# Optimization experiments

Measured on AMD Instinct MI355X. Metric: run time of the kernel, lower is better.

Reference implementation:

```python
import jax, jax.numpy as jnp
import numpy as np

EPS = 1e-5
NEG = -10000.0


def rel_shift(x):
    # x: [B, H, T1, T2] with T2 = 2*T1 - 1 -> returns [B, H, T1, T1]
    B, H, T1, T2 = x.shape
    x = jnp.pad(x, ((0, 0), (0, 0), (0, 0), (1, 0)))        # [B,H,T1,T2+1]
    x = x.reshape(B, H, T2 + 1, T1)[:, :, 1:, :].reshape(B, H, T1, T2)
    return x[:, :, :, : T2 // 2 + 1]


def setup_inputs() -> dict:
    key = jax.random.key(0)
    B, C, T, H = 4, 512, 1024, 8
    ks = jax.random.split(key, 16)
    s = 0.02
    inp = {
        "x": jax.random.normal(ks[0], (B, C, T), jnp.float32),
        "pos_emb": jax.random.normal(ks[1], (1, C, 2 * T - 1), jnp.float32),
        "x_mask": jnp.ones((B, 1, T), jnp.float32),
        "gamma": jnp.ones((C,), jnp.float32),
        "beta": jnp.zeros((C,), jnp.float32),
        "Wq": jax.random.normal(ks[2], (C, C), jnp.float32) * s,
        "bq": jnp.zeros((C,), jnp.float32),
        "Wk": jax.random.normal(ks[3], (C, C), jnp.float32) * s,
        "bk": jnp.zeros((C,), jnp.float32),
        "Wv": jax.random.normal(ks[4], (C, C), jnp.float32) * s,
        "bv": jnp.zeros((C,), jnp.float32),
        "Wp": jax.random.normal(ks[5], (C, C), jnp.float32) * s,
        "u_bias": jax.random.normal(ks[6], (H, C // H), jnp.float32) * s,
        "v_bias": jax.random.normal(ks[7], (H, C // H), jnp.float32) * s,
        "Wo": jax.random.normal(ks[8], (C, C), jnp.float32) * s,
        "bo": jnp.zeros((C,), jnp.float32),
    }
    return inp


def reference(x, pos_emb, x_mask, gamma, beta, Wq, bq, Wk, bk, Wv, bv, Wp,
              u_bias, v_bias, Wo, bo):
    B, C, T = x.shape
    H, Dh = u_bias.shape

    # channel LayerNorm (axis=1)
    mean = jnp.mean(x, axis=1, keepdims=True)
    var = jnp.mean((x - mean) ** 2, axis=1, keepdims=True)
    xn = (x - mean) * jax.lax.rsqrt(var + EPS)
    xn = xn * gamma[None, :, None] + beta[None, :, None]

    conv1x1 = lambda W, b, z: jnp.einsum('oc,bct->bot', W, z) + b[None, :, None]
    q = conv1x1(Wq, bq, xn).reshape(B, H, Dh, T)
    k = conv1x1(Wk, bk, xn).reshape(B, H, Dh, T)
    v = conv1x1(Wv, bv, xn).reshape(B, H, Dh, T)
    p = jnp.einsum('oc,xct->xot', Wp, pos_emb)          # [1, C, 2T-1], no bias
    p = p.reshape(p.shape[0], H, Dh, -1)[0]             # [H, Dh, 2T-1]

    content = jnp.einsum('bhdt,bhds->bhts', q + u_bias[None, :, :, None], k)
    pos = jnp.einsum('bhdt,hds->bhts', q + v_bias[None, :, :, None], p)
    pos = rel_shift(pos)                                 # [B, H, T, T]

    score = (content + pos) / jnp.sqrt(jnp.float32(C))
    attn_mask = x_mask[:, :, None, :] * x_mask[:, :, :, None]  # [B,1,T,T]
    score = jnp.where(attn_mask == 0, NEG, score)
    attn = jax.nn.softmax(score, axis=-1)

    # context[d,t] = sum_s v[d,s] * attn[s,t]
    ctx = jnp.einsum('bhds,bhst->bhdt', v, attn).reshape(B, C, T)
    return jnp.einsum('oc,bct->bot', Wo, ctx) + bo[None, :, None]
```

## Files before the change

kernel.cpp:

```cpp
#include <hip/hip_runtime.h>
#include <hip/hip_bf16.h>
#include <cmath>

typedef unsigned short u16;
typedef __bf16 bf16_t;
typedef bf16_t bf16x8 __attribute__((ext_vector_type(8)));
typedef float f32x4 __attribute__((ext_vector_type(4)));
typedef u16 u16x8 __attribute__((ext_vector_type(8)));

#define MFMA16(A,B,C) __builtin_amdgcn_mfma_f32_16x16x32_bf16(A,B,C,0,0,0)

#define CB 512
#define TT 1024
#define NH 8
#define DH 64
#define ALPHA (0.044194173824159216f * 1.4426950408889634f)
#define MASKL 14426.950408889634f

static __device__ __forceinline__ u16 f2b(float f) {
  unsigned u = __float_as_uint(f);
  unsigned r = u + 0x7FFFu + ((u >> 16) & 1u);
  return (u16)(r >> 16);
}
static __device__ __forceinline__ float b2f(u16 u) {
  return __uint_as_float(((unsigned)u) << 16);
}
static __device__ __forceinline__ bf16x8 ldb8(const u16* p) {
  return *reinterpret_cast<const bf16x8*>(p);
}

__global__ __launch_bounds__(256)
void convert5(const float* __restrict__ Wq, const float* __restrict__ Wk,
              const float* __restrict__ Wv, const float* __restrict__ Wp,
              const float* __restrict__ Wo,
              u16* __restrict__ Wstk, u16* __restrict__ WoB)
{
  int i = blockIdx.x * 256 + threadIdx.x;
  int sel = i >> 15, loc = i & 32767;
  const float* src = (sel == 0) ? Wq : (sel == 1) ? Wk : (sel == 2) ? Wv
                   : (sel == 3) ? Wp : Wo;
  const float4 a = ((const float4*)src)[loc * 2 + 0];
  const float4 b = ((const float4*)src)[loc * 2 + 1];
  u16x8 o;
  o[0] = f2b(a.x); o[1] = f2b(a.y); o[2] = f2b(a.z); o[3] = f2b(a.w);
  o[4] = f2b(b.x); o[5] = f2b(b.y); o[6] = f2b(b.z); o[7] = f2b(b.w);
  u16* dst = (sel < 4) ? (Wstk + (size_t)i * 8) : (WoB + (size_t)loc * 8);
  *(u16x8*)dst = o;
}

__global__ __launch_bounds__(256)
void transpose_pe(const float* __restrict__ pe, u16* __restrict__ posT)
{
  __shared__ float tile[64][65];
  int j0 = blockIdx.x * 64, c0 = blockIdx.y * 64;
  for (int e = threadIdx.x; e < 4096; e += 256) {
    int cc = e >> 6, jj = e & 63;
    int j = j0 + jj;
    tile[jj][cc] = (j < 2047) ? pe[(size_t)(c0 + cc) * 2047 + j] : 0.f;
  }
  __syncthreads();
  for (int e = threadIdx.x; e < 4096; e += 256) {
    int jj = e >> 6, cc = e & 63;
    posT[(size_t)(j0 + jj) * 512 + c0 + cc] = f2b(tile[jj][cc]);
  }
}

__global__ __launch_bounds__(256)
void ln_kernel(const float* __restrict__ x, const float* __restrict__ gamma,
               const float* __restrict__ beta, u16* __restrict__ xnT)
{
  __shared__ float sred[8][33], ssred[8][33];
  int tl = threadIdx.x & 31, cg = threadIdx.x >> 5;
  int t = blockIdx.x * 32 + tl;
  int b = blockIdx.y;
  const float* xb = x + (size_t)b * CB * TT + t;
  float s = 0.f, ss = 0.f;
  for (int c = cg * 64; c < cg * 64 + 64; ++c) {
    float v = xb[(size_t)c * TT];
    s += v; ss += v * v;
  }
  sred[cg][tl] = s; ssred[cg][tl] = ss;
  __syncthreads();
  float S = 0.f, SS = 0.f;
  #pragma unroll
  for (int g = 0; g < 8; ++g) { S += sred[g][tl]; SS += ssred[g][tl]; }
  float mean = S * (1.f / 512.f);
  float var = SS * (1.f / 512.f) - mean * mean;
  float rstd = rsqrtf(var + 1e-5f);
  u16* orow = xnT + ((size_t)b * TT + t) * CB;
  for (int c8 = 0; c8 < 8; ++c8) {
    int c = cg * 64 + c8 * 8;
    u16x8 o;
    #pragma unroll
    for (int j = 0; j < 8; ++j) {
      float v = xb[(size_t)(c + j) * TT];
      o[j] = f2b((v - mean) * rstd * gamma[c + j] + beta[c + j]);
    }
    *(u16x8*)(orow + c) = o;
  }
}

template<int K, int OMODE>
__global__ __launch_bounds__(256)
void gemm2(const u16* __restrict__ A, const u16* __restrict__ XT,
           long xStride, long oStride, int Nout,
           const float* __restrict__ b0, void* __restrict__ outv)
{
  const int tid = threadIdx.x, w = tid >> 6, lane = tid & 63;
  const int ln16 = lane & 15, kg = lane >> 4;
  const int wm = w & 1, wn = w >> 1;
  const int m0 = blockIdx.y * 64 + wm * 32;
  const int n0 = blockIdx.x * 128 + wn * 64;
  const int z = blockIdx.z;
  const u16* Ar = A + (size_t)(m0 + ln16) * K + kg * 8;
  const u16* Br = XT + (size_t)z * xStride + (size_t)(n0 + ln16) * K + kg * 8;
  f32x4 acc[2][4] = {};
  #pragma unroll 2
  for (int ks = 0; ks < K / 32; ++ks) {
    bf16x8 a[2], bb[4];
    #pragma unroll
    for (int mt = 0; mt < 2; ++mt) a[mt] = ldb8(Ar + (size_t)mt * 16 * K + ks * 32);
    #pragma unroll
    for (int nt = 0; nt < 4; ++nt) bb[nt] = ldb8(Br + (size_t)nt * 16 * K + ks * 32);
    #pragma unroll
    for (int mt = 0; mt < 2; ++mt)
      #pragma unroll
      for (int nt = 0; nt < 4; ++nt)
        acc[mt][nt] = MFMA16(a[mt], bb[nt], acc[mt][nt]);
  }
  float add[2][4];
  #pragma unroll
  for (int mt = 0; mt < 2; ++mt)
    #pragma unroll
    for (int jr = 0; jr < 4; ++jr)
      add[mt][jr] = b0 ? b0[m0 + mt * 16 + kg * 4 + jr] : 0.f;
  #pragma unroll
  for (int mt = 0; mt < 2; ++mt)
    #pragma unroll
    for (int nt = 0; nt < 4; ++nt) {
      const int n = n0 + nt * 16 + ln16;
      if constexpr (OMODE == 0) {
        float* out = (float*)outv;
        #pragma unroll
        for (int jr = 0; jr < 4; ++jr)
          out[(size_t)z * oStride + (size_t)(m0 + mt * 16 + kg * 4 + jr) * Nout + n] =
              acc[mt][nt][jr] + add[mt][jr];
      } else {
        const int m_low = m0 + mt * 16;
        const size_t o = (size_t)z * oStride +
                         ((size_t)(m_low >> 6) * Nout + n) * 64 + (m_low & 63) + kg * 4;
        ushort4 s4;
        s4.x = f2b(acc[mt][nt][0] + add[mt][0]);
        s4.y = f2b(acc[mt][nt][1] + add[mt][1]);
        s4.z = f2b(acc[mt][nt][2] + add[mt][2]);
        s4.w = f2b(acc[mt][nt][3] + add[mt][3]);
        *reinterpret_cast<ushort4*>((u16*)outv + o) = s4;
      }
    }
}

__global__ __launch_bounds__(256)
void gemm3_out(const u16* __restrict__ A, const u16* __restrict__ XT,
               const float* __restrict__ b0, float* __restrict__ out)
{
  const int tid = threadIdx.x, w = tid >> 6, lane = tid & 63;
  const int ln16 = lane & 15, kg = lane >> 4;
  const int m0 = blockIdx.y * 64 + (w & 1) * 32;
  const int n0 = blockIdx.x * 64 + (w >> 1) * 32;
  const int z = blockIdx.z;
  const u16* Ar = A + (size_t)(m0 + ln16) * 512 + kg * 8;
  const u16* Br = XT + (size_t)z * (512 * 1024) + (size_t)(n0 + ln16) * 512 + kg * 8;
  f32x4 acc[2][2] = {};
  #pragma unroll 2
  for (int ks = 0; ks < 16; ++ks) {
    bf16x8 a[2], bb[2];
    #pragma unroll
    for (int mt = 0; mt < 2; ++mt) a[mt] = ldb8(Ar + (size_t)mt * 16 * 512 + ks * 32);
    #pragma unroll
    for (int nt = 0; nt < 2; ++nt) bb[nt] = ldb8(Br + (size_t)nt * 16 * 512 + ks * 32);
    #pragma unroll
    for (int mt = 0; mt < 2; ++mt)
      #pragma unroll
      for (int nt = 0; nt < 2; ++nt)
        acc[mt][nt] = MFMA16(a[mt], bb[nt], acc[mt][nt]);
  }
  #pragma unroll
  for (int mt = 0; mt < 2; ++mt) {
    float add[4];
    #pragma unroll
    for (int jr = 0; jr < 4; ++jr)
      add[jr] = b0[m0 + mt * 16 + kg * 4 + jr];
    #pragma unroll
    for (int nt = 0; nt < 2; ++nt) {
      const int n = n0 + nt * 16 + ln16;
      #pragma unroll
      for (int jr = 0; jr < 4; ++jr)
        out[(size_t)z * (512 * 1024) + (size_t)(m0 + mt * 16 + kg * 4 + jr) * 1024 + n] =
            acc[mt][nt][jr] + add[jr];
    }
  }
}

__global__ __launch_bounds__(256)
void proj_qkv2(const u16* __restrict__ Wstk, const u16* __restrict__ xnT,
               const float* __restrict__ bq, const float* __restrict__ ub,
               const float* __restrict__ bk, const float* __restrict__ bv,
               u16* __restrict__ quB, u16* __restrict__ kB, u16* __restrict__ vB)
{
  const int tid = threadIdx.x, w = tid >> 6, lane = tid & 63;
  const int ln16 = lane & 15, kg = lane >> 4;
  const int wm = w & 1, wn = w >> 1;
  const int my = blockIdx.y;
  const int sec = my >> 3;
  const int m0l = (my & 7) * 64 + wm * 32;
  const int n0 = blockIdx.x * 128 + wn * 64;
  const int z = blockIdx.z;
  const long XS = (long)TT * CB;
  const long QS = (long)NH * TT * DH;
  const u16* Ar = Wstk + (size_t)(sec * 512 + m0l + ln16) * 512 + kg * 8;
  const u16* Br = xnT + (size_t)z * XS + (size_t)(n0 + ln16) * 512 + kg * 8;
  f32x4 acc[2][4] = {};
  #pragma unroll 2
  for (int ks = 0; ks < 16; ++ks) {
    bf16x8 a[2], bb[4];
    #pragma unroll
    for (int mt = 0; mt < 2; ++mt) a[mt] = ldb8(Ar + (size_t)mt * 16 * 512 + ks * 32);
    #pragma unroll
    for (int nt = 0; nt < 4; ++nt) bb[nt] = ldb8(Br + (size_t)nt * 16 * 512 + ks * 32);
    #pragma unroll
    for (int mt = 0; mt < 2; ++mt)
      #pragma unroll
      for (int nt = 0; nt < 4; ++nt)
        acc[mt][nt] = MFMA16(a[mt], bb[nt], acc[mt][nt]);
  }
  const float scl = (sec == 0) ? ALPHA : 1.f;
  float add[2][4];
  #pragma unroll
  for (int mt = 0; mt < 2; ++mt)
    #pragma unroll
    for (int jr = 0; jr < 4; ++jr) {
      int m = m0l + mt * 16 + kg * 4 + jr;
      add[mt][jr] = (sec == 0) ? (bq[m] + ub[m]) : (sec == 1) ? bk[m] : bv[m];
    }
  if (sec < 2) {
    u16* dst = sec ? kB : quB;
    #pragma unroll
    for (int mt = 0; mt < 2; ++mt)
      #pragma unroll
      for (int nt = 0; nt < 4; ++nt) {
        const int n = n0 + nt * 16 + ln16;
        const int m_low = m0l + mt * 16;
        const size_t o = (size_t)z * QS +
                         ((size_t)(m_low >> 6) * TT + n) * 64 + (m_low & 63) + kg * 4;
        ushort4 s4;
        s4.x = f2b((acc[mt][nt][0] + add[mt][0]) * scl);
        s4.y = f2b((acc[mt][nt][1] + add[mt][1]) * scl);
        s4.z = f2b((acc[mt][nt][2] + add[mt][2]) * scl);
        s4.w = f2b((acc[mt][nt][3] + add[mt][3]) * scl);
        *reinterpret_cast<ushort4*>(dst + o) = s4;
      }
  } else {
    #pragma unroll
    for (int mt = 0; mt < 2; ++mt)
      #pragma unroll
      for (int nt = 0; nt < 4; ++nt) {
        const int n = n0 + nt * 16 + ln16;
        #pragma unroll
        for (int jr = 0; jr < 4; ++jr)
          vB[(size_t)z * QS + (size_t)(m0l + mt * 16 + kg * 4 + jr) * TT + n] =
              f2b(acc[mt][nt][jr] + add[mt][jr]);
      }
  }
}

__global__ __launch_bounds__(256)
void corr_kernel(const u16* __restrict__ pp, const float* __restrict__ ub,
                 const float* __restrict__ vb, float* __restrict__ corr)
{
  const int h = blockIdx.y;
  const int j = blockIdx.x * 256 + threadIdx.x;
  __shared__ float dl[64];
  if (threadIdx.x < 64)
    dl[threadIdx.x] = vb[h * 64 + threadIdx.x] - ub[h * 64 + threadIdx.x];
  __syncthreads();
  const u16* prow = pp + ((size_t)h * 2048 + j) * 64;
  float s = 0.f;
  #pragma unroll
  for (int d8 = 0; d8 < 8; ++d8) {
    union { bf16x8 v; u16 u[8]; } pu;
    pu.v = ldb8(prow + d8 * 8);
    #pragma unroll
    for (int e = 0; e < 8; ++e) s += b2f(pu.u[e]) * dl[d8 * 8 + e];
  }
  corr[h * 2048 + j] = s * ALPHA;
}

__global__ __launch_bounds__(256)
void stats_mfma(const u16* __restrict__ qu, const u16* __restrict__ kk_,
                const u16* __restrict__ pp, const float* __restrict__ corr,
                const float* __restrict__ xmask, float* __restrict__ ls)
{
  const int tid = threadIdx.x;
  const int w = tid >> 6, lane = tid & 63;
  const int ln16 = lane & 15, kg = lane >> 4;
  const int bid = blockIdx.x;
  const int bh = (bid & 7) + 8 * ((bid >> 3) & 3);
  const int rest = bid >> 5;
  const int qi0 = (rest & 31) * 32;
  const int part = rest >> 5;
  const int b = bh >> 3, h = bh & 7;
  const u16* quP = qu + (size_t)bh * TT * DH;
  const u16* kP  = kk_ + (size_t)bh * TT * DH;
  const u16* pP  = pp + (size_t)h * 2048 * DH;
  const float* corrP = corr + (h << 11);

  __shared__ u16 G[4][32][100];
  __shared__ float red[4][32];

  bf16x8 qa[2][2];
  #pragma unroll
  for (int mt = 0; mt < 2; ++mt)
    #pragma unroll
    for (int kc = 0; kc < 2; ++kc)
      qa[mt][kc] = ldb8(&quP[(size_t)(qi0 + mt * 16 + ln16) * DH + kc * 32 + kg * 8]);
  float aq[2][4];
  #pragma unroll
  for (int mt = 0; mt < 2; ++mt)
    #pragma unroll
    for (int jr = 0; jr < 4; ++jr)
      aq[mt][jr] = (xmask[b * TT + qi0 + mt * 16 + kg * 4 + jr] - 1.f) * MASKL;

  float rs[2][4] = {};
  for (int c = 0; c < 2; ++c) {
    const int ki0 = (part * 8 + c * 4 + w) * 64;
    const int j0 = ki0 - qi0 + 992;
    #pragma unroll
    for (int nt = 0; nt < 6; ++nt) {
      const size_t po = (size_t)(j0 + nt * 16 + ln16) * DH + kg * 8;
      bf16x8 pb0 = ldb8(&pP[po]);
      bf16x8 pb1 = ldb8(&pP[po + 32]);
      const float cval = corrP[j0 + nt * 16 + ln16];
      #pragma unroll
      for (int mt = 0; mt < 2; ++mt) {
        f32x4 g = {0.f, 0.f, 0.f, 0.f};
        g = MFMA16(qa[mt][0], pb0, g);
        g = MFMA16(qa[mt][1], pb1, g);
        #pragma unroll
        for (int jr = 0; jr < 4; ++jr)
          G[w][mt * 16 + kg * 4 + jr][nt * 16 + ln16] = f2b(g[jr] + cval);
      }
    }
    #pragma unroll
    for (int nt = 0; nt < 4; ++nt) {
      const size_t ko = (size_t)(ki0 + nt * 16 + ln16) * DH + kg * 8;
      bf16x8 kb0 = ldb8(&kP[ko]);
      bf16x8 kb1 = ldb8(&kP[ko + 32]);
      const float ak = (xmask[b * TT + ki0 + nt * 16 + ln16] - 1.f) * MASKL;
      #pragma unroll
      for (int mt = 0; mt < 2; ++mt) {
        f32x4 dd = { aq[mt][0] + ak, aq[mt][1] + ak, aq[mt][2] + ak, aq[mt][3] + ak };
        dd = MFMA16(qa[mt][0], kb0, dd);
        dd = MFMA16(qa[mt][1], kb1, dd);
        #pragma unroll
        for (int jr = 0; jr < 4; ++jr) {
          const int qrow = mt * 16 + kg * 4 + jr;
          const int u = nt * 16 + ln16 - qrow + 31;
          rs[mt][jr] += exp2f(dd[jr] + b2f(G[w][qrow][u]));
        }
      }
    }
  }
  #pragma unroll
  for (int mt = 0; mt < 2; ++mt)
    #pragma unroll
    for (int jr = 0; jr < 4; ++jr) {
      float v = rs[mt][jr];
      v += __shfl_xor(v, 1); v += __shfl_xor(v, 2);
      v += __shfl_xor(v, 4); v += __shfl_xor(v, 8);
      rs[mt][jr] = v;
    }
  if (ln16 == 0) {
    #pragma unroll
    for (int mt = 0; mt < 2; ++mt)
      #pragma unroll
      for (int jr = 0; jr < 4; ++jr)
        red[w][mt * 16 + kg * 4 + jr] = rs[mt][jr];
  }
  __syncthreads();
  if (tid < 32)
    ls[(size_t)part * 32768 + (size_t)bh * TT + qi0 + tid] =
        red[0][tid] + red[1][tid] + red[2][tid] + red[3][tid];
}

__global__ __launch_bounds__(256)
void ctx_mfma(const u16* __restrict__ qu, const u16* __restrict__ kk_,
              const u16* __restrict__ vv, const u16* __restrict__ pp,
              const float* __restrict__ corr, const float* __restrict__ xmask,
              u16* __restrict__ ctx2)
{
  const int tid = threadIdx.x;
  const int w = tid >> 6, lane = tid & 63;
  const int ln16 = lane & 15, kg = lane >> 4;
  const int l48 = lane & 48;
  const int bid = blockIdx.x;
  const int bh = (bid & 7) + 8 * ((bid >> 3) & 3);
  const int rest = bid >> 5;
  const int t0 = (rest & 15) * 64;
  const int part = rest >> 4;
  const int b = bh >> 3, h = bh & 7;
  const u16* quP = qu + (size_t)bh * TT * DH;
  const u16* kP  = kk_ + (size_t)bh * TT * DH;
  const u16* vP  = vv + (size_t)bh * DH * TT;
  const u16* pP  = pp + (size_t)h * 2048 * DH;
  const float* corrP = corr + (h << 11);

  __shared__ __align__(16) u16 P[2][64][72];

  bf16x8 ka[4][2];
  #pragma unroll
  for (int nt = 0; nt < 4; ++nt)
    #pragma unroll
    for (int kc = 0; kc < 2; ++kc)
      ka[nt][kc] = ldb8(&kP[(size_t)(t0 + nt * 16 + ln16) * DH + kc * 32 + kg * 8]);
  float at4[4];
  #pragma unroll
  for (int nt = 0; nt < 4; ++nt)
    at4[nt] = (xmask[b * TT + t0 + nt * 16 + ln16] - 1.f) * MASKL;

  auto scores = [&](int qcn, int buf) {
    const int qw = qcn * 64 + w * 16;
    const int j0 = t0 - qw + 1008;
    const size_t qo = (size_t)(qw + ln16) * DH + kg * 8;
    bf16x8 qa0 = ldb8(&quP[qo]), qa1 = ldb8(&quP[qo + 32]);
    f32x4 g[5];
    #pragma unroll
    for (int n = 0; n < 5; ++n) {
      const size_t po = (size_t)(j0 + n * 16 + ln16) * DH + kg * 8;
      bf16x8 pb0 = ldb8(&pP[po]), pb1 = ldb8(&pP[po + 32]);
      const float cval = corrP[j0 + n * 16 + ln16];
      f32x4 t = {cval, cval, cval, cval};
      t = MFMA16(qa0, pb0, t);
      t = MFMA16(qa1, pb1, t);
      g[n] = t;
    }
    float sg[4][5];
    #pragma unroll
    for (int jr = 0; jr < 4; ++jr) {
      const int qrow = kg * 4 + jr;
      const int src = l48 | ((ln16 + 15 - qrow) & 15);
      #pragma unroll
      for (int n = 0; n < 5; ++n) sg[jr][n] = __shfl(g[n][jr], src);
    }
    float aqv[4];
    #pragma unroll
    for (int jr = 0; jr < 4; ++jr)
      aqv[jr] = (xmask[b * TT + qw + kg * 4 + jr] - 1.f) * MASKL;
    #pragma unroll
    for (int nt = 0; nt < 4; ++nt) {
      f32x4 dd = { aqv[0] + at4[nt], aqv[1] + at4[nt],
                   aqv[2] + at4[nt], aqv[3] + at4[nt] };
      dd = MFMA16(qa0, ka[nt][0], dd);
      dd = MFMA16(qa1, ka[nt][1], dd);
      unsigned lo = 0, hi = 0;
      #pragma unroll
      for (int jr = 0; jr < 4; ++jr) {
        const int qrow = kg * 4 + jr;
        const float val = (ln16 <= qrow) ? sg[jr][nt] : sg[jr][nt + 1];
        const float e = exp2f(dd[jr] + val);
        const unsigned bb = f2b(e);
        if (jr == 0) lo = bb; else if (jr == 1) lo |= bb << 16;
        else if (jr == 2) hi = bb; else hi |= bb << 16;
      }
      *reinterpret_cast<uint2*>(&P[buf][nt * 16 + ln16][w * 16 + kg * 4]) =
          make_uint2(lo, hi);
    }
  };

  f32x4 cacc[4] = {};
  scores(part * 4, 0);
  __syncthreads();
  #pragma unroll
  for (int i = 0; i < 4; ++i) {
    const int qc = part * 4 + i;
    const size_t vbase = (size_t)(w * 16 + ln16) * TT + qc * 64 + kg * 8;
    bf16x8 vf0 = ldb8(&vP[vbase]), vf1 = ldb8(&vP[vbase + 32]);
    #pragma unroll
    for (int nt = 0; nt < 4; ++nt) {
      bf16x8 pb0 = *reinterpret_cast<const bf16x8*>(&P[i & 1][nt * 16 + ln16][kg * 8]);
      bf16x8 pb1 = *reinterpret_cast<const bf16x8*>(&P[i & 1][nt * 16 + ln16][32 + kg * 8]);
      cacc[nt] = MFMA16(vf0, pb0, cacc[nt]);
      cacc[nt] = MFMA16(vf1, pb1, cacc[nt]);
    }
    if (i < 3) {
      scores(qc + 1, (i + 1) & 1);
      __syncthreads();
    }
  }
  #pragma unroll
  for (int nt = 0; nt < 4; ++nt) {
    const int t = t0 + nt * 16 + ln16;
    ushort4 s4;
    s4.x = f2b(cacc[nt][0]); s4.y = f2b(cacc[nt][1]);
    s4.z = f2b(cacc[nt][2]); s4.w = f2b(cacc[nt][3]);
    *reinterpret_cast<ushort4*>(
      &ctx2[((size_t)b * TT + t) * 2048 + part * 512 + h * 64 + w * 16 + kg * 4]) = s4;
  }
}

__global__ __launch_bounds__(256)
void vscale(u16* __restrict__ vv, const float* __restrict__ ls)
{
  int i = blockIdx.x * 256 + threadIdx.x;
  int bh = i >> 13;
  int rem = i & 8191;
  int d = rem >> 7;
  int qi0 = (rem & 127) * 8;
  const float* lsP = ls + bh * 1024 + qi0;
  u16* row = vv + ((size_t)bh * 64 + d) * 1024 + qi0;
  union { u16x8 v; u16 u[8]; } t;
  t.v = *(u16x8*)row;
  u16x8 o;
  #pragma unroll
  for (int e = 0; e < 8; ++e) {
    float linv = __builtin_amdgcn_rcpf(lsP[e] + lsP[32768 + e]);
    o[e] = f2b(b2f(t.u[e]) * linv);
  }
  *(u16x8*)row = o;
}

__global__ __launch_bounds__(256)
void reduce_ctx(const u16* __restrict__ ctx2, u16* __restrict__ ctxS)
{
  int i = blockIdx.x * 256 + threadIdx.x;
  int row = i >> 6;
  int c0 = (i & 63) * 8;
  const u16* src = ctx2 + (size_t)row * 2048 + c0;
  float s[8] = {};
  #pragma unroll
  for (int p = 0; p < 4; ++p) {
    union { u16x8 v; u16 u[8]; } t;
    t.v = *(const u16x8*)(src + p * 512);
    #pragma unroll
    for (int e = 0; e < 8; ++e) s[e] += b2f(t.u[e]);
  }
  u16x8 o;
  #pragma unroll
  for (int e = 0; e < 8; ++e) o[e] = f2b(s[e]);
  *(u16x8*)(ctxS + (size_t)row * 512 + c0) = o;
}

extern "C" void kernel_launch(void* const* d_in, const int* in_sizes, int n_in,
                              void* d_out, int out_size, void* d_ws, size_t ws_size,
                              hipStream_t stream)
{
  (void)in_sizes; (void)n_in; (void)out_size;
  const float* x     = (const float*)d_in[0];
  const float* pe    = (const float*)d_in[1];
  const float* xm    = (const float*)d_in[2];
  const float* gamma = (const float*)d_in[3];
  const float* beta  = (const float*)d_in[4];
  const float* Wq    = (const float*)d_in[5];
  const float* bq    = (const float*)d_in[6];
  const float* Wk    = (const float*)d_in[7];
  const float* bk    = (const float*)d_in[8];
  const float* Wv    = (const float*)d_in[9];
  const float* bv    = (const float*)d_in[10];
  const float* Wp    = (const float*)d_in[11];
  const float* ub    = (const float*)d_in[12];
  const float* vb    = (const float*)d_in[13];
  const float* Wo    = (const float*)d_in[14];
  const float* bo    = (const float*)d_in[15];

  char* ws = (char*)d_ws;
  u16*  quB  = (u16*) (ws + 0);
  u16*  ctxS = (u16*) (ws + 0);
  u16*  kB   = (u16*) (ws + 4194304);
  u16*  vB   = (u16*) (ws + 8388608);
  u16*  pB   = (u16*) (ws + 12582912);
  float* corrB = (float*)(ws + 14680064);
  float* lsB = (float*)(ws + 14745600);
  u16*  WoB  = (u16*) (ws + 15007744);
  u16*  ctx2 = (u16*) (ws + 15532032);
  u16*  xnT  = (u16*) (ws + 15532032);
  u16*  posT = (u16*) (ws + 19726336);
  u16*  Wstk = (u16*) (ws + 21823488);
  if (ws_size < 32309248) return;

  dim3 blk(256);

  convert5<<<dim3(640), blk, 0, stream>>>(Wq, Wk, Wv, Wp, Wo, Wstk, WoB);
  transpose_pe<<<dim3(32, 8), blk, 0, stream>>>(pe, posT);
  ln_kernel<<<dim3(32, 4), blk, 0, stream>>>(x, gamma, beta, xnT);

  proj_qkv2<<<dim3(8, 24, 4), blk, 0, stream>>>(Wstk, xnT, bq, ub, bk, bv, quB, kB, vB);
  gemm2<512, 1><<<dim3(16, 8, 1), blk, 0, stream>>>(
      Wstk + (size_t)1536 * 512, posT, 0, 0, 2048, nullptr, pB);
  corr_kernel<<<dim3(8, 8), blk, 0, stream>>>(pB, ub, vb, corrB);

  stats_mfma<<<dim3(2048), blk, 0, stream>>>(quB, kB, pB, corrB, xm, lsB);
  vscale<<<dim3(1024), blk, 0, stream>>>(vB, lsB);
  ctx_mfma<<<dim3(2048), blk, 0, stream>>>(quB, kB, vB, pB, corrB, xm, ctx2);
  reduce_ctx<<<dim3(1024), blk, 0, stream>>>(ctx2, ctxS);

  gemm3_out<<<dim3(16, 8, 4), blk, 0, stream>>>(WoB, ctxS, bo, (float*)d_out);
}
```

Before: 214.3 us.

## Use native bf16 pack conversions, swap GEMM tilings for pos and output projections, raise MFMA priority

Replaces the manual round-to-nearest float-to-bf16 bit trick with compiler bf16 casts, including a paired two-value pack so the hardware packed-convert instruction can be used. The 32x32-per-wave GEMM template is now used for the positional projection with a doubled grid, and the 32x64 GEMM template for the output projection with a halved grid. It also raises wave priority around the PV MFMA block in ctx_mfma. These changes target conversion ALU cost in the score and epilogue paths and tile-versus-occupancy balance in the two GEMMs, and they may change rounding behaviour slightly for NaN or edge values.

```diff
diff --git a/kernel.cpp b/kernel.cpp
--- a/kernel.cpp
+++ b/kernel.cpp
@@ -5,6 +5,7 @@
 typedef unsigned short u16;
 typedef __bf16 bf16_t;
 typedef bf16_t bf16x8 __attribute__((ext_vector_type(8)));
+typedef bf16_t bf16x2 __attribute__((ext_vector_type(2)));
 typedef float f32x4 __attribute__((ext_vector_type(4)));
 typedef u16 u16x8 __attribute__((ext_vector_type(8)));
 
@@ -18,9 +19,11 @@
 #define MASKL 14426.950408889634f
 
 static __device__ __forceinline__ u16 f2b(float f) {
-  unsigned u = __float_as_uint(f);
-  unsigned r = u + 0x7FFFu + ((u >> 16) & 1u);
-  return (u16)(r >> 16);
+  union { bf16_t b; u16 u; } r; r.b = (bf16_t)f; return r.u;
+}
+static __device__ __forceinline__ unsigned cvt2(float lo, float hi) {
+  union { bf16x2 v; unsigned u; } r;
+  r.v[0] = (bf16_t)lo; r.v[1] = (bf16_t)hi; return r.u;
 }
 static __device__ __forceinline__ float b2f(u16 u) {
   return __uint_as_float(((unsigned)u) << 16);
@@ -149,56 +152,68 @@
         const int m_low = m0 + mt * 16;
         const size_t o = (size_t)z * oStride +
                          ((size_t)(m_low >> 6) * Nout + n) * 64 + (m_low & 63) + kg * 4;
-        ushort4 s4;
-        s4.x = f2b(acc[mt][nt][0] + add[mt][0]);
-        s4.y = f2b(acc[mt][nt][1] + add[mt][1]);
-        s4.z = f2b(acc[mt][nt][2] + add[mt][2]);
-        s4.w = f2b(acc[mt][nt][3] + add[mt][3]);
-        *reinterpret_cast<ushort4*>((u16*)outv + o) = s4;
+        uint2 o2;
+        o2.x = cvt2(acc[mt][nt][0] + add[mt][0], acc[mt][nt][1] + add[mt][1]);
+        o2.y = cvt2(acc[mt][nt][2] + add[mt][2], acc[mt][nt][3] + add[mt][3]);
+        *reinterpret_cast<uint2*>((u16*)outv + o) = o2;
       }
     }
 }
 
-__global__ __launch_bounds__(256)
-void gemm3_out(const u16* __restrict__ A, const u16* __restrict__ XT,
-               const float* __restrict__ b0, float* __restrict__ out)
+template<int K, int OMODE>
+__global__ __launch_bounds__(256)
+void gemm3(const u16* __restrict__ A, const u16* __restrict__ XT,
+           long xStride, long oStride, int Nout,
+           const float* __restrict__ b0, void* __restrict__ outv)
 {
   const int tid = threadIdx.x, w = tid >> 6, lane = tid & 63;
   const int ln16 = lane & 15, kg = lane >> 4;
   const int m0 = blockIdx.y * 64 + (w & 1) * 32;
   const int n0 = blockIdx.x * 64 + (w >> 1) * 32;
   const int z = blockIdx.z;
-  const u16* Ar = A + (size_t)(m0 + ln16) * 512 + kg * 8;
-  const u16* Br = XT + (size_t)z * (512 * 1024) + (size_t)(n0 + ln16) * 512 + kg * 8;
+  const u16* Ar = A + (size_t)(m0 + ln16) * K + kg * 8;
+  const u16* Br = XT + (size_t)z * xStride + (size_t)(n0 + ln16) * K + kg * 8;
   f32x4 acc[2][2] = {};
   #pragma unroll 2
-  for (int ks = 0; ks < 16; ++ks) {
+  for (int ks = 0; ks < K / 32; ++ks) {
     bf16x8 a[2], bb[2];
     #pragma unroll
-    for (int mt = 0; mt < 2; ++mt) a[mt] = ldb8(Ar + (size_t)mt * 16 * 512 + ks * 32);
-    #pragma unroll
-    for (int nt = 0; nt < 2; ++nt) bb[nt] = ldb8(Br + (size_t)nt * 16 * 512 + ks * 32);
+    for (int mt = 0; mt < 2; ++mt) a[mt] = ldb8(Ar + (size_t)mt * 16 * K + ks * 32);
+    #pragma unroll
+    for (int nt = 0; nt < 2; ++nt) bb[nt] = ldb8(Br + (size_t)nt * 16 * K + ks * 32);
     #pragma unroll
     for (int mt = 0; mt < 2; ++mt)
       #pragma unroll
       for (int nt = 0; nt < 2; ++nt)
         acc[mt][nt] = MFMA16(a[mt], bb[nt], acc[mt][nt]);
   }
-  #pragma unroll
-  for (int mt = 0; mt < 2; ++mt) {
-    float add[4];
+  float add[2][4];
+  #pragma unroll
+  for (int mt = 0; mt < 2; ++mt)
     #pragma unroll
     for (int jr = 0; jr < 4; ++jr)
-      add[jr] = b0[m0 + mt * 16 + kg * 4 + jr];
+      add[mt][jr] = b0 ? b0[m0 + mt * 16 + kg * 4 + jr] : 0.f;
+  #pragma unroll
+  for (int mt = 0; mt < 2; ++mt)
     #pragma unroll
     for (int nt = 0; nt < 2; ++nt) {
       const int n = n0 + nt * 16 + ln16;
-      #pragma unroll
-      for (int jr = 0; jr < 4; ++jr)
-        out[(size_t)z * (512 * 1024) + (size_t)(m0 + mt * 16 + kg * 4 + jr) * 1024 + n] =
-            acc[mt][nt][jr] + add[jr];
-    }
-  }
+      if constexpr (OMODE == 0) {
+        float* out = (float*)outv;
+        #pragma unroll
+        for (int jr = 0; jr < 4; ++jr)
+          out[(size_t)z * oStride + (size_t)(m0 + mt * 16 + kg * 4 + jr) * Nout + n] =
+              acc[mt][nt][jr] + add[mt][jr];
+      } else {
+        const int m_low = m0 + mt * 16;
+        const size_t o = (size_t)z * oStride +
+                         ((size_t)(m_low >> 6) * Nout + n) * 64 + (m_low & 63) + kg * 4;
+        uint2 o2;
+        o2.x = cvt2(acc[mt][nt][0] + add[mt][0], acc[mt][nt][1] + add[mt][1]);
+        o2.y = cvt2(acc[mt][nt][2] + add[mt][2], acc[mt][nt][3] + add[mt][3]);
+        *reinterpret_cast<uint2*>((u16*)outv + o) = o2;
+      }
+    }
 }
 
 __global__ __launch_bounds__(256)
@@ -252,12 +267,12 @@
         const int m_low = m0l + mt * 16;
         const size_t o = (size_t)z * QS +
                          ((size_t)(m_low >> 6) * TT + n) * 64 + (m_low & 63) + kg * 4;
-        ushort4 s4;
-        s4.x = f2b((acc[mt][nt][0] + add[mt][0]) * scl);
-        s4.y = f2b((acc[mt][nt][1] + add[mt][1]) * scl);
-        s4.z = f2b((acc[mt][nt][2] + add[mt][2]) * scl);
-        s4.w = f2b((acc[mt][nt][3] + add[mt][3]) * scl);
-        *reinterpret_cast<ushort4*>(dst + o) = s4;
+        uint2 o2;
+        o2.x = cvt2((acc[mt][nt][0] + add[mt][0]) * scl,
+                    (acc[mt][nt][1] + add[mt][1]) * scl);
+        o2.y = cvt2((acc[mt][nt][2] + add[mt][2]) * scl,
+                    (acc[mt][nt][3] + add[mt][3]) * scl);
+        *reinterpret_cast<uint2*>(dst + o) = o2;
       }
   } else {
     #pragma unroll
@@ -461,18 +476,17 @@
                    aqv[2] + at4[nt], aqv[3] + at4[nt] };
       dd = MFMA16(qa0, ka[nt][0], dd);
       dd = MFMA16(qa1, ka[nt][1], dd);
-      unsigned lo = 0, hi = 0;
+      float ev[4];
       #pragma unroll
       for (int jr = 0; jr < 4; ++jr) {
         const int qrow = kg * 4 + jr;
         const float val = (ln16 <= qrow) ? sg[jr][nt] : sg[jr][nt + 1];
-        const float e = exp2f(dd[jr] + val);
-        const unsigned bb = f2b(e);
-        if (jr == 0) lo = bb; else if (jr == 1) lo |= bb << 16;
-        else if (jr == 2) hi = bb; else hi |= bb << 16;
+        ev[jr] = exp2f(dd[jr] + val);
       }
-      *reinterpret_cast<uint2*>(&P[buf][nt * 16 + ln16][w * 16 + kg * 4]) =
-          make_uint2(lo, hi);
+      uint2 o2;
+      o2.x = cvt2(ev[0], ev[1]);
+      o2.y = cvt2(ev[2], ev[3]);
+      *reinterpret_cast<uint2*>(&P[buf][nt * 16 + ln16][w * 16 + kg * 4]) = o2;
     }
   };
 
@@ -484,6 +498,7 @@
     const int qc = part * 4 + i;
     const size_t vbase = (size_t)(w * 16 + ln16) * TT + qc * 64 + kg * 8;
     bf16x8 vf0 = ldb8(&vP[vbase]), vf1 = ldb8(&vP[vbase + 32]);
+    __builtin_amdgcn_s_setprio(1);
     #pragma unroll
     for (int nt = 0; nt < 4; ++nt) {
       bf16x8 pb0 = *reinterpret_cast<const bf16x8*>(&P[i & 1][nt * 16 + ln16][kg * 8]);
@@ -491,6 +506,7 @@
       cacc[nt] = MFMA16(vf0, pb0, cacc[nt]);
       cacc[nt] = MFMA16(vf1, pb1, cacc[nt]);
     }
+    __builtin_amdgcn_s_setprio(0);
     if (i < 3) {
       scores(qc + 1, (i + 1) & 1);
       __syncthreads();
@@ -499,11 +515,11 @@
   #pragma unroll
   for (int nt = 0; nt < 4; ++nt) {
     const int t = t0 + nt * 16 + ln16;
-    ushort4 s4;
-    s4.x = f2b(cacc[nt][0]); s4.y = f2b(cacc[nt][1]);
-    s4.z = f2b(cacc[nt][2]); s4.w = f2b(cacc[nt][3]);
-    *reinterpret_cast<ushort4*>(
-      &ctx2[((size_t)b * TT + t) * 2048 + part * 512 + h * 64 + w * 16 + kg * 4]) = s4;
+    uint2 o2;
+    o2.x = cvt2(cacc[nt][0], cacc[nt][1]);
+    o2.y = cvt2(cacc[nt][2], cacc[nt][3]);
+    *reinterpret_cast<uint2*>(
+      &ctx2[((size_t)b * TT + t) * 2048 + part * 512 + h * 64 + w * 16 + kg * 4]) = o2;
   }
 }
 
@@ -593,7 +609,7 @@
   ln_kernel<<<dim3(32, 4), blk, 0, stream>>>(x, gamma, beta, xnT);
 
   proj_qkv2<<<dim3(8, 24, 4), blk, 0, stream>>>(Wstk, xnT, bq, ub, bk, bv, quB, kB, vB);
-  gemm2<512, 1><<<dim3(16, 8, 1), blk, 0, stream>>>(
+  gemm3<512, 1><<<dim3(32, 8, 1), blk, 0, stream>>>(
       Wstk + (size_t)1536 * 512, posT, 0, 0, 2048, nullptr, pB);
   corr_kernel<<<dim3(8, 8), blk, 0, stream>>>(pB, ub, vb, corrB);
 
@@ -602,5 +618,6 @@
   ctx_mfma<<<dim3(2048), blk, 0, stream>>>(quB, kB, vB, pB, corrB, xm, ctx2);
   reduce_ctx<<<dim3(1024), blk, 0, stream>>>(ctx2, ctxS);
 
-  gemm3_out<<<dim3(16, 8, 4), blk, 0, stream>>>(WoB, ctxS, bo, (float*)d_out);
-}
+  gemm2<512, 0><<<dim3(8, 8, 4), blk, 0, stream>>>(
+      WoB, ctxS, (long)TT * CB, (long)CB * TT, TT, bo, (float*)d_out);
+}
```

New measurement: 206.9 us. 1.04x faster.
